# Kernel tuning notes

Hardware: AMD Instinct MI355X
Metric: run time of the kernel (lower is better)

## Reference

```python
import jax, jax.numpy as jnp
import numpy as np

EMBED = 2048
N_HEAD = 32
N_KV = 8
HEAD_DIM = 64
GROUP = N_HEAD // N_KV


def _rope_tables(seq_len, head_dim):
    inv_freq = 1.0 / (10000.0 ** (jnp.arange(0, head_dim, 2, dtype=jnp.float32) / head_dim))
    ang = jnp.arange(seq_len, dtype=jnp.float32)[:, None] * inv_freq[None, :]  # [S, D/2]
    ang = jnp.concatenate([ang, ang], axis=-1)  # [S, D]
    return jnp.cos(ang), jnp.sin(ang)


def apply_rope(x, cos, sin, offset=0):
    # x: [B, H, S, D]
    S, D = x.shape[2], x.shape[3]
    x1, x2 = x[..., : D // 2], x[..., D // 2 :]
    c = cos[offset : offset + S][None, None]
    s = sin[offset : offset + S][None, None]
    rotated = jnp.concatenate([-x2, x1], axis=-1)
    return (x * c + rotated * s).astype(x.dtype)


def setup_inputs() -> dict:
    key = jax.random.key(0)
    kx, kq, kk, kv, ko = jax.random.split(key, 5)
    B, S = 2, 2048
    x = jax.random.normal(kx, (B, S, EMBED), dtype=jnp.float32)
    mask = jnp.triu(jnp.ones((S, S), dtype=bool), k=1)  # causal: True = masked
    cos, sin = _rope_tables(S, HEAD_DIM)
    std = 0.02
    Wq = jax.random.normal(kq, (EMBED, EMBED), dtype=jnp.float32) * std
    Wk = jax.random.normal(kk, (EMBED, N_KV * HEAD_DIM), dtype=jnp.float32) * std
    Wv = jax.random.normal(kv, (EMBED, N_KV * HEAD_DIM), dtype=jnp.float32) * std
    Wo = jax.random.normal(ko, (EMBED, EMBED), dtype=jnp.float32) * std
    return {"x": x, "mask": mask, "cos": cos, "sin": sin,
            "Wq": Wq, "Wk": Wk, "Wv": Wv, "Wo": Wo}


def reference(x, mask, cos, sin, Wq, Wk, Wv, Wo):
    B, S, E = x.shape
    # projections (no bias)
    q = (x @ Wq).reshape(B, S, N_HEAD, HEAD_DIM).transpose(0, 2, 1, 3)  # [B,H,S,D]
    k = (x @ Wk).reshape(B, S, N_KV, HEAD_DIM).transpose(0, 2, 1, 3)    # [B,G,S,D]
    v = (x @ Wv).reshape(B, S, N_KV, HEAD_DIM).transpose(0, 2, 1, 3)    # [B,G,S,D]
    q = apply_rope(q, cos, sin, offset=0)
    k = apply_rope(k, cos, sin, offset=0)
    next_k, next_v = k, v  # kv cache to return
    # GQA: head h uses kv group h // GROUP; avoid repeat_interleave via reshape
    qg = q.reshape(B, N_KV, GROUP, S, HEAD_DIM)
    scores = jnp.einsum('bgjsd,bgtd->bgjst', qg, k) / np.float32(np.sqrt(HEAD_DIM))
    scores = jnp.where(mask[None, None, None], -jnp.inf, scores)
    attn = jax.nn.softmax(scores, axis=-1)
    out = jnp.einsum('bgjst,bgtd->bgjsd', attn, v)          # [B,G,group,S,D]
    out = out.reshape(B, N_HEAD, S, HEAD_DIM).transpose(0, 2, 1, 3).reshape(B, S, E)
    return out @ Wo, next_k, next_v
```

## Files before the change

kernel.cpp:

```cpp
#include <hip/hip_runtime.h>
#include <hip/hip_bf16.h>
#include <math.h>

#define NH 32
#define NKV 8
#define HD 64
#define B_ 2
#define S_ 2048
#define E_ 2048
#define M_ 4096

typedef unsigned short ushort_t;
typedef __attribute__((ext_vector_type(8))) short short8;
typedef __attribute__((ext_vector_type(4))) short short4v;
typedef __attribute__((ext_vector_type(4))) float floatx4;

__device__ inline unsigned short f2bf(float f) {
  unsigned int u = __float_as_uint(f);
  return (unsigned short)((u + 0x7FFFu + ((u >> 16) & 1u)) >> 16);
}

__device__ inline float fexp2(float x) {
  float r;
  asm("v_exp_f32 %0, %1" : "=v"(r) : "v"(x));
  return r;
}

__device__ inline void ld_lds16(const void* g, void* l) {
  __builtin_amdgcn_global_load_lds((__attribute__((address_space(1))) void*)g,
                                   (__attribute__((address_space(3))) void*)l, 16, 0, 0);
}

__global__ __launch_bounds__(256) void cast_x(const float* __restrict__ x,
                                              ushort_t* __restrict__ xb) {
  size_t i = ((size_t)blockIdx.x * 256 + threadIdx.x) * 8;
  float4 a = *(const float4*)(x + i);
  float4 b = *(const float4*)(x + i + 4);
  short8 o;
  o[0] = (short)f2bf(a.x); o[1] = (short)f2bf(a.y);
  o[2] = (short)f2bf(a.z); o[3] = (short)f2bf(a.w);
  o[4] = (short)f2bf(b.x); o[5] = (short)f2bf(b.y);
  o[6] = (short)f2bf(b.z); o[7] = (short)f2bf(b.w);
  *(short8*)(xb + i) = o;
}

__global__ __launch_bounds__(256) void transpose_w(const float* __restrict__ in,
                                                   ushort_t* __restrict__ out,
                                                   int R, int C) {
  __shared__ float tile[32][33];
  int c0 = blockIdx.x * 32, r0 = blockIdx.y * 32;
  int x = threadIdx.x, y0 = threadIdx.y;
  for (int i = 0; i < 4; i++) {
    int r = y0 + i * 8;
    tile[r][x] = in[(size_t)(r0 + r) * C + c0 + x];
  }
  __syncthreads();
  for (int i = 0; i < 4; i++) {
    int r = y0 + i * 8;
    out[(size_t)(c0 + r) * R + r0 + x] = f2bf(tile[x][r]);
  }
}

__global__ __launch_bounds__(256) void transpose_v(const float* __restrict__ outv,
                                                   ushort_t* __restrict__ vt) {
  __shared__ float t64[64][65];
  int bg = blockIdx.y;
  int tt = blockIdx.x;
  int s0 = tt * 64;
  int tid = threadIdx.x;
  size_t ibase = (size_t)bg * S_ * HD + (size_t)s0 * HD;
  for (int i = tid; i < 1024; i += 256) {
    int sr = i >> 4, dc = (i & 15) * 4;
    float4 v = *(const float4*)(outv + ibase + (size_t)sr * HD + dc);
    t64[sr][dc] = v.x; t64[sr][dc + 1] = v.y; t64[sr][dc + 2] = v.z; t64[sr][dc + 3] = v.w;
  }
  __syncthreads();
  size_t obase = ((size_t)bg * 32 + tt) * 4096;
  for (int i = tid; i < 512; i += 256) {
    int d = i >> 3, ss = (i & 7) * 8;
    short8 o;
#pragma unroll
    for (int e = 0; e < 8; e++) o[e] = (short)f2bf(t64[ss + e][d]);
    *(short8*)(vt + obase + d * 64 + (ss ^ ((d & 7) << 3))) = o;
  }
}

__device__ __forceinline__ void gemm128_core(const ushort_t* __restrict__ Ag,
                                             const ushort_t* __restrict__ Bg,
                                             floatx4 (&acc)[4][4]) {
  __shared__ __align__(16) ushort_t As[2][128][64];
  __shared__ __align__(16) ushort_t Bs[2][128][64];
  int tid = threadIdx.x;
  int w = tid >> 6, lane = tid & 63;
  int wm = (w >> 1) * 64, wn = (w & 1) * 64;
  int lr = lane & 15, quad = lane >> 4;
  int sx = lr & 7;
  char* Asb = (char*)As;
  char* Bsb = (char*)Bs;

  size_t so[4];
#pragma unroll
  for (int s = 0; s < 4; s++)
    so[s] = (size_t)(w * 32 + s * 8 + (lane >> 3)) * 4096 + (size_t)(((lane & 7) ^ (lane >> 3)) * 16);
  const char* abase = (const char*)Ag;
  const char* bbase = (const char*)Bg;

#define STAGE128(buf, kt)                                          \
  do {                                                             \
    size_t ko = (size_t)(kt) * 128;                                \
    char* Ad = Asb + (buf) * 16384 + w * 4096;                     \
    char* Bd = Bsb + (buf) * 16384 + w * 4096;                     \
    _Pragma("unroll") for (int s = 0; s < 4; s++) {                \
      ld_lds16(abase + so[s] + ko, Ad + s * 1024);                 \
      ld_lds16(bbase + so[s] + ko, Bd + s * 1024);                 \
    }                                                              \
  } while (0)

  STAGE128(0, 0);
  __syncthreads();

  int cur = 0;
  for (int kt = 0; kt < 32; kt++) {
    if (kt < 31) STAGE128(cur ^ 1, kt + 1);
    const char* Ab = Asb + cur * 16384;
    const char* Bb = Bsb + cur * 16384;
    short8 af[4][2], bfr[4][2];
#pragma unroll
    for (int i = 0; i < 4; i++) {
      size_t rb = (size_t)(wm + i * 16 + lr) * 128;
#pragma unroll
      for (int ks = 0; ks < 2; ks++)
        af[i][ks] = *(const short8*)(Ab + rb + (((ks * 4 + quad) ^ sx) << 4));
    }
#pragma unroll
    for (int j = 0; j < 4; j++) {
      size_t rb = (size_t)(wn + j * 16 + lr) * 128;
#pragma unroll
      for (int ks = 0; ks < 2; ks++)
        bfr[j][ks] = *(const short8*)(Bb + rb + (((ks * 4 + quad) ^ sx) << 4));
    }
#pragma unroll
    for (int i = 0; i < 4; i++)
#pragma unroll
      for (int j = 0; j < 4; j++) {
        acc[i][j] = __builtin_amdgcn_mfma_f32_16x16x32_bf16(af[i][0], bfr[j][0], acc[i][j], 0, 0, 0);
        acc[i][j] = __builtin_amdgcn_mfma_f32_16x16x32_bf16(af[i][1], bfr[j][1], acc[i][j], 0, 0, 0);
      }
    __syncthreads();
    cur ^= 1;
  }
#undef STAGE128
}

__global__ __launch_bounds__(256) void gemm_qkv(const ushort_t* __restrict__ xb,
                                                const ushort_t* __restrict__ WT,
                                                ushort_t* __restrict__ qbf,
                                                float* __restrict__ outk,
                                                ushort_t* __restrict__ kbf,
                                                float* __restrict__ outv,
                                                const float* __restrict__ cosP,
                                                const float* __restrict__ sinP) {
  int o = blockIdx.y * 24 + blockIdx.x;
  int swz = (o & 7) * 96 + (o >> 3);
  int n0 = (swz % 24) * 128, m0 = (swz / 24) * 128;
  int tid = threadIdx.x;
  int w = tid >> 6, lane = tid & 63;
  int wm = (w >> 1) * 64, wn = (w & 1) * 64;
  int lr = lane & 15, quad = lane >> 4;

  floatx4 acc[4][4] = {};
  gemm128_core(xb + (size_t)m0 * 2048, WT + (size_t)n0 * 2048, acc);

  if (n0 < 2048) {
    const float QS = 0.125f * 1.4426950408889634f;
#pragma unroll
    for (int i = 0; i < 4; i++)
#pragma unroll
      for (int j = 0; j < 2; j++) {
        int d = j * 16 + lr;
#pragma unroll
        for (int r = 0; r < 4; r++) {
          int row = m0 + wm + i * 16 + quad * 4 + r;
          int s = row & (S_ - 1);
          float c = cosP[s * 64 + d], sn = sinP[s * 64 + d];
          float x1 = acc[i][j][r], x2 = acc[i][j + 2][r];
          size_t oo = (size_t)row * 2048 + n0 + wn + d;
          qbf[oo] = f2bf((x1 * c - x2 * sn) * QS);
          qbf[oo + 32] = f2bf((x2 * c + x1 * sn) * QS);
        }
      }
  } else if (n0 < 2560) {
    int h = (n0 - 2048 + wn) >> 6;
#pragma unroll
    for (int i = 0; i < 4; i++)
#pragma unroll
      for (int j = 0; j < 2; j++) {
        int d = j * 16 + lr;
#pragma unroll
        for (int r = 0; r < 4; r++) {
          int row = m0 + wm + i * 16 + quad * 4 + r;
          int s = row & (S_ - 1), b = row >> 11;
          float c = cosP[s * 64 + d], sn = sinP[s * 64 + d];
          float x1 = acc[i][j][r], x2 = acc[i][j + 2][r];
          float y1 = x1 * c - x2 * sn, y2 = x2 * c + x1 * sn;
          size_t rowb = ((size_t)(b * NKV + h) * S_ + s) * 64;
          int xr = (s & 7) << 3;
          outk[rowb + d] = y1; outk[rowb + d + 32] = y2;
          kbf[rowb + (d ^ xr)] = f2bf(y1);
          kbf[rowb + ((d + 32) ^ xr)] = f2bf(y2);
        }
      }
  } else {
    int h = (n0 - 2560 + wn) >> 6;
#pragma unroll
    for (int i = 0; i < 4; i++)
#pragma unroll
      for (int j = 0; j < 4; j++) {
        int d = j * 16 + lr;
#pragma unroll
        for (int r = 0; r < 4; r++) {
          int row = m0 + wm + i * 16 + quad * 4 + r;
          int s = row & (S_ - 1), b = row >> 11;
          outv[((size_t)(b * NKV + h) * S_ + s) * 64 + d] = acc[i][j][r];
        }
      }
  }
}

__global__ __launch_bounds__(256) void gemm_o(const ushort_t* __restrict__ ctx,
                                              const ushort_t* __restrict__ WoT,
                                              float* __restrict__ y) {
  int o = blockIdx.y * 16 + blockIdx.x;
  int swz = (o & 7) * 64 + (o >> 3);
  int n0 = (swz % 16) * 128, m0 = (swz / 16) * 128;
  int tid = threadIdx.x;
  int w = tid >> 6, lane = tid & 63;
  int wm = (w >> 1) * 64, wn = (w & 1) * 64;
  int lr = lane & 15, quad = lane >> 4;

  floatx4 acc[4][4] = {};
  gemm128_core(ctx + (size_t)m0 * 2048, WoT + (size_t)n0 * 2048, acc);

#pragma unroll
  for (int i = 0; i < 4; i++)
#pragma unroll
    for (int j = 0; j < 4; j++) {
      int row = m0 + wm + i * 16 + quad * 4;
      int col = n0 + wn + j * 16 + lr;
#pragma unroll
      for (int r = 0; r < 4; r++)
        y[(size_t)(row + r) * 2048 + col] = acc[i][j][r];
    }
}

__global__ __launch_bounds__(256, 4) void attn2(ushort_t* __restrict__ q,
                                                const ushort_t* __restrict__ k,
                                                const ushort_t* __restrict__ vt) {
  __shared__ __align__(16) ushort_t KV[2][2][64][64];
  __shared__ __align__(16) ushort_t Ps[4][16][64];
  int bh = blockIdx.x;
  int qt = 31 - blockIdx.y;
  int b = bh >> 5, h = bh & 31, g = h >> 2;
  int tid = threadIdx.x;
  int w = tid >> 6, lane = tid & 63;
  int lr = lane & 15, quad = lane >> 4;

  int qg = qt * 64 + w * 16 + lr;
  short8 aq0, aq1;
  {
    const ushort_t* qp = q + ((size_t)(b * S_ + qg) * NH + h) * HD;
    aq0 = *(const short8*)(qp + quad * 8);
    aq1 = *(const short8*)(qp + 32 + quad * 8);
  }
  floatx4 od[4] = {};
  float mi = -INFINITY, li = 0.f;

  const char* ksrc = (const char*)(k + (size_t)(b * NKV + g) * S_ * HD) + w * 2048 + lane * 16;
  const char* vsrc = (const char*)(vt + (size_t)(b * NKV + g) * S_ * HD) + w * 2048 + lane * 16;
  char* dB = (char*)&KV[0][0][0][0] + w * 2048;

  int sw = (lr & 7) << 4;
  int ro0 = (quad * 16) ^ sw;
  int ro1 = (64 + quad * 16) ^ sw;
  char* Pw = (char*)&Ps[0][0][0] + w * 2048;

  ld_lds16(ksrc, dB);
  ld_lds16(ksrc + 1024, dB + 1024);
  ld_lds16(vsrc, dB + 8192);
  ld_lds16(vsrc + 1024, dB + 8192 + 1024);
  asm volatile("s_waitcnt vmcnt(0)" ::: "memory");
  __syncthreads();

  int cur = 0;
  for (int t = 0; t <= qt; t++) {
    if (t < qt) {
      const char* kn = ksrc + (size_t)(t + 1) * 8192;
      const char* vn = vsrc + (size_t)(t + 1) * 8192;
      char* d = dB + (cur ^ 1) * 16384;
      ld_lds16(kn, d); ld_lds16(kn + 1024, d + 1024);
      ld_lds16(vn, d + 8192); ld_lds16(vn + 1024, d + 8192 + 1024);
    }
    const char* Kb = (const char*)&KV[cur][0][0][0];
    const char* Vb = (const char*)&KV[cur][1][0][0];
    floatx4 sc[4];
#pragma unroll
    for (int kn = 0; kn < 4; kn++) {
      short8 a0 = *(const short8*)(Kb + (kn * 16 + lr) * 128 + ro0);
      short8 a1 = *(const short8*)(Kb + (kn * 16 + lr) * 128 + ro1);
      floatx4 c = {};
      c = __builtin_amdgcn_mfma_f32_16x16x32_bf16(a0, aq0, c, 0, 0, 0);
      c = __builtin_amdgcn_mfma_f32_16x16x32_bf16(a1, aq1, c, 0, 0, 0);
      sc[kn] = c;
    }
    float pv[16];
#pragma unroll
    for (int kn = 0; kn < 4; kn++)
#pragma unroll
      for (int r = 0; r < 4; r++) pv[kn * 4 + r] = sc[kn][r];
    if (t == qt) {
#pragma unroll
      for (int e = 0; e < 16; e++) {
        int kg = t * 64 + (e >> 2) * 16 + quad * 4 + (e & 3);
        if (kg > qg) pv[e] = -INFINITY;
      }
    }
    float mx = pv[0];
#pragma unroll
    for (int e = 1; e < 16; e++) mx = fmaxf(mx, pv[e]);
    mx = fmaxf(mx, __shfl_xor(mx, 16));
    mx = fmaxf(mx, __shfl_xor(mx, 32));
    if (__any(mx > mi + 11.5f)) {
      float mn = fmaxf(mi, mx);
      float al = fexp2(mi - mn);
      li *= al;
#pragma unroll
      for (int dn = 0; dn < 4; dn++) {
        od[dn][0] *= al; od[dn][1] *= al; od[dn][2] *= al; od[dn][3] *= al;
      }
      mi = mn;
    }
    float ps = 0.f;
#pragma unroll
    for (int e = 0; e < 16; e++) {
      pv[e] = fexp2(pv[e] - mi);
      ps += pv[e];
    }
    ps += __shfl_xor(ps, 16);
    ps += __shfl_xor(ps, 32);
    li += ps;
#pragma unroll
    for (int kn = 0; kn < 4; kn++) {
      unsigned int u0, u1;
      asm("v_cvt_pk_bf16_f32 %0, %1, %2" : "=v"(u0) : "v"(pv[kn * 4 + 0]), "v"(pv[kn * 4 + 1]));
      asm("v_cvt_pk_bf16_f32 %0, %1, %2" : "=v"(u1) : "v"(pv[kn * 4 + 2]), "v"(pv[kn * 4 + 3]));
      uint2 uu; uu.x = u0; uu.y = u1;
      *(uint2*)(Pw + lr * 128 + ((kn * 32 + quad * 8) ^ sw)) = uu;
    }
    short8 pb0 = *(const short8*)(Pw + lr * 128 + ro0);
    short8 pb1 = *(const short8*)(Pw + lr * 128 + ro1);
#pragma unroll
    for (int dn = 0; dn < 4; dn++) {
      short8 va = *(const short8*)(Vb + (dn * 16 + lr) * 128 + ro0);
      short8 vb = *(const short8*)(Vb + (dn * 16 + lr) * 128 + ro1);
      od[dn] = __builtin_amdgcn_mfma_f32_16x16x32_bf16(va, pb0, od[dn], 0, 0, 0);
      od[dn] = __builtin_amdgcn_mfma_f32_16x16x32_bf16(vb, pb1, od[dn], 0, 0, 0);
    }
    asm volatile("s_waitcnt vmcnt(0)" ::: "memory");
    __syncthreads();
    cur ^= 1;
  }
  float inv = 1.f / li;
  ushort_t* outp = q + ((size_t)(b * S_ + qg) * NH + h) * HD;
#pragma unroll
  for (int dn = 0; dn < 4; dn++) {
    short4v u;
    u[0] = (short)f2bf(od[dn][0] * inv); u[1] = (short)f2bf(od[dn][1] * inv);
    u[2] = (short)f2bf(od[dn][2] * inv); u[3] = (short)f2bf(od[dn][3] * inv);
    *(short4v*)(outp + dn * 16 + quad * 4) = u;
  }
}

extern "C" void kernel_launch(void* const* d_in, const int* in_sizes, int n_in,
                              void* d_out, int out_size, void* d_ws, size_t ws_size,
                              hipStream_t stream) {
  const float* x = (const float*)d_in[0];
  const float* cosT = (const float*)d_in[2];
  const float* sinT = (const float*)d_in[3];
  const float* Wq = (const float*)d_in[4];
  const float* Wk = (const float*)d_in[5];
  const float* Wv = (const float*)d_in[6];
  const float* Wo = (const float*)d_in[7];

  char* ws = (char*)d_ws;
  ushort_t* WT = (ushort_t*)(ws);
  ushort_t* WoT = (ushort_t*)(ws + 12582912);
  ushort_t* xb = (ushort_t*)(ws + 20971520);
  ushort_t* qbf = (ushort_t*)(ws + 37748736);
  ushort_t* kbf = (ushort_t*)(ws + 54525952);
  ushort_t* vt = (ushort_t*)(ws + 58720256);

  float* y = (float*)d_out;
  float* outk = y + (size_t)M_ * E_;
  float* outv = outk + (size_t)B_ * NKV * S_ * HD;

  cast_x<<<dim3(4096), 256, 0, stream>>>(x, xb);
  transpose_w<<<dim3(64, 64), dim3(32, 8), 0, stream>>>(Wq, WT, 2048, 2048);
  transpose_w<<<dim3(16, 64), dim3(32, 8), 0, stream>>>(Wk, WT + 2048 * 2048, 2048, 512);
  transpose_w<<<dim3(16, 64), dim3(32, 8), 0, stream>>>(Wv, WT + 2560 * 2048, 2048, 512);
  transpose_w<<<dim3(64, 64), dim3(32, 8), 0, stream>>>(Wo, WoT, 2048, 2048);

  gemm_qkv<<<dim3(24, 32), 256, 0, stream>>>(xb, WT, qbf, outk, kbf, outv, cosT, sinT);
  transpose_v<<<dim3(32, 16), 256, 0, stream>>>(outv, vt);

  attn2<<<dim3(64, 32), 256, 0, stream>>>(qbf, kbf, vt);

  gemm_o<<<dim3(16, 32), 256, 0, stream>>>(qbf, WoT, y);
}
```

Measured before the change: 344.0 us.

## Merge prep kernels into one launch, regroup GEMM tiles per XCD, prioritize attention MFMAs

Fuses the x cast and the four weight transposes into a single prep kernel with a flat block index, removing four kernel launches and their gaps. Remaps GEMM tile indices so each XCD gets a contiguous 8xN block of output tiles, which is meant to improve L2 reuse of A and B panels. It also raises wave priority around the MFMA sections in the attention kernel to favour matrix issue over other waves. The changes are independent. The tile remap assumes grid sizes that divide evenly across the XCD groups.

After: 322.2 us. 1.07x faster.

```diff
diff --git a/kernel.cpp b/kernel.cpp
--- a/kernel.cpp
+++ b/kernel.cpp
@@ -31,25 +31,10 @@
                                    (__attribute__((address_space(3))) void*)l, 16, 0, 0);
 }
 
-__global__ __launch_bounds__(256) void cast_x(const float* __restrict__ x,
-                                              ushort_t* __restrict__ xb) {
-  size_t i = ((size_t)blockIdx.x * 256 + threadIdx.x) * 8;
-  float4 a = *(const float4*)(x + i);
-  float4 b = *(const float4*)(x + i + 4);
-  short8 o;
-  o[0] = (short)f2bf(a.x); o[1] = (short)f2bf(a.y);
-  o[2] = (short)f2bf(a.z); o[3] = (short)f2bf(a.w);
-  o[4] = (short)f2bf(b.x); o[5] = (short)f2bf(b.y);
-  o[6] = (short)f2bf(b.z); o[7] = (short)f2bf(b.w);
-  *(short8*)(xb + i) = o;
-}
-
-__global__ __launch_bounds__(256) void transpose_w(const float* __restrict__ in,
-                                                   ushort_t* __restrict__ out,
-                                                   int R, int C) {
-  __shared__ float tile[32][33];
-  int c0 = blockIdx.x * 32, r0 = blockIdx.y * 32;
-  int x = threadIdx.x, y0 = threadIdx.y;
+__device__ inline void transp32(const float* __restrict__ in, ushort_t* __restrict__ out,
+                                int R, int C, int bx, int by, int tid, float (*tile)[33]) {
+  int c0 = bx * 32, r0 = by * 32;
+  int x = tid & 31, y0 = tid >> 5;
   for (int i = 0; i < 4; i++) {
     int r = y0 + i * 8;
     tile[r][x] = in[(size_t)(r0 + r) * C + c0 + x];
@@ -59,6 +44,38 @@
     int r = y0 + i * 8;
     out[(size_t)(c0 + r) * R + r0 + x] = f2bf(tile[x][r]);
   }
+}
+
+__global__ __launch_bounds__(256) void prep(const float* __restrict__ x,
+                                            ushort_t* __restrict__ xb,
+                                            const float* __restrict__ Wq,
+                                            const float* __restrict__ Wk,
+                                            const float* __restrict__ Wv,
+                                            const float* __restrict__ Wo,
+                                            ushort_t* __restrict__ WT,
+                                            ushort_t* __restrict__ WoT) {
+  __shared__ float tile[32][33];
+  int bid = blockIdx.x, tid = threadIdx.x;
+  if (bid < 4096) {
+    size_t i = ((size_t)bid * 256 + tid) * 8;
+    float4 a = *(const float4*)(x + i);
+    float4 b = *(const float4*)(x + i + 4);
+    short8 o;
+    o[0] = (short)f2bf(a.x); o[1] = (short)f2bf(a.y);
+    o[2] = (short)f2bf(a.z); o[3] = (short)f2bf(a.w);
+    o[4] = (short)f2bf(b.x); o[5] = (short)f2bf(b.y);
+    o[6] = (short)f2bf(b.z); o[7] = (short)f2bf(b.w);
+    *(short8*)(xb + i) = o;
+    return;
+  }
+  bid -= 4096;
+  if (bid < 4096) { transp32(Wq, WT, 2048, 2048, bid & 63, bid >> 6, tid, tile); return; }
+  bid -= 4096;
+  if (bid < 1024) { transp32(Wk, WT + 2048 * 2048, 2048, 512, bid & 15, bid >> 4, tid, tile); return; }
+  bid -= 1024;
+  if (bid < 1024) { transp32(Wv, WT + 2560 * 2048, 2048, 512, bid & 15, bid >> 4, tid, tile); return; }
+  bid -= 1024;
+  transp32(Wo, WoT, 2048, 2048, bid & 63, bid >> 6, tid, tile);
 }
 
 __global__ __launch_bounds__(256) void transpose_v(const float* __restrict__ outv,
@@ -161,8 +178,10 @@
                                                 const float* __restrict__ cosP,
                                                 const float* __restrict__ sinP) {
   int o = blockIdx.y * 24 + blockIdx.x;
-  int swz = (o & 7) * 96 + (o >> 3);
-  int n0 = (swz % 24) * 128, m0 = (swz / 24) * 128;
+  int xcd = o & 7, i = o >> 3;
+  int mg = xcd >> 1, ng = xcd & 1;
+  int m0 = (mg * 8 + i / 12) * 128;
+  int n0 = (ng * 12 + i % 12) * 128;
   int tid = threadIdx.x;
   int w = tid >> 6, lane = tid & 63;
   int wm = (w >> 1) * 64, wn = (w & 1) * 64;
@@ -174,16 +193,16 @@
   if (n0 < 2048) {
     const float QS = 0.125f * 1.4426950408889634f;
 #pragma unroll
-    for (int i = 0; i < 4; i++)
+    for (int i2 = 0; i2 < 4; i2++)
 #pragma unroll
       for (int j = 0; j < 2; j++) {
         int d = j * 16 + lr;
 #pragma unroll
         for (int r = 0; r < 4; r++) {
-          int row = m0 + wm + i * 16 + quad * 4 + r;
+          int row = m0 + wm + i2 * 16 + quad * 4 + r;
           int s = row & (S_ - 1);
           float c = cosP[s * 64 + d], sn = sinP[s * 64 + d];
-          float x1 = acc[i][j][r], x2 = acc[i][j + 2][r];
+          float x1 = acc[i2][j][r], x2 = acc[i2][j + 2][r];
           size_t oo = (size_t)row * 2048 + n0 + wn + d;
           qbf[oo] = f2bf((x1 * c - x2 * sn) * QS);
           qbf[oo + 32] = f2bf((x2 * c + x1 * sn) * QS);
@@ -192,16 +211,16 @@
   } else if (n0 < 2560) {
     int h = (n0 - 2048 + wn) >> 6;
 #pragma unroll
-    for (int i = 0; i < 4; i++)
+    for (int i2 = 0; i2 < 4; i2++)
 #pragma unroll
       for (int j = 0; j < 2; j++) {
         int d = j * 16 + lr;
 #pragma unroll
         for (int r = 0; r < 4; r++) {
-          int row = m0 + wm + i * 16 + quad * 4 + r;
+          int row = m0 + wm + i2 * 16 + quad * 4 + r;
           int s = row & (S_ - 1), b = row >> 11;
           float c = cosP[s * 64 + d], sn = sinP[s * 64 + d];
-          float x1 = acc[i][j][r], x2 = acc[i][j + 2][r];
+          float x1 = acc[i2][j][r], x2 = acc[i2][j + 2][r];
           float y1 = x1 * c - x2 * sn, y2 = x2 * c + x1 * sn;
           size_t rowb = ((size_t)(b * NKV + h) * S_ + s) * 64;
           int xr = (s & 7) << 3;
@@ -213,15 +232,15 @@
   } else {
     int h = (n0 - 2560 + wn) >> 6;
 #pragma unroll
-    for (int i = 0; i < 4; i++)
+    for (int i2 = 0; i2 < 4; i2++)
 #pragma unroll
       for (int j = 0; j < 4; j++) {
         int d = j * 16 + lr;
 #pragma unroll
         for (int r = 0; r < 4; r++) {
-          int row = m0 + wm + i * 16 + quad * 4 + r;
+          int row = m0 + wm + i2 * 16 + quad * 4 + r;
           int s = row & (S_ - 1), b = row >> 11;
-          outv[((size_t)(b * NKV + h) * S_ + s) * 64 + d] = acc[i][j][r];
+          outv[((size_t)(b * NKV + h) * S_ + s) * 64 + d] = acc[i2][j][r];
         }
       }
   }
@@ -231,8 +250,10 @@
                                               const ushort_t* __restrict__ WoT,
                                               float* __restrict__ y) {
   int o = blockIdx.y * 16 + blockIdx.x;
-  int swz = (o & 7) * 64 + (o >> 3);
-  int n0 = (swz % 16) * 128, m0 = (swz / 16) * 128;
+  int xcd = o & 7, i = o >> 3;
+  int mg = xcd >> 1, ng = xcd & 1;
+  int m0 = (mg * 8 + (i >> 3)) * 128;
+  int n0 = (ng * 8 + (i & 7)) * 128;
   int tid = threadIdx.x;
   int w = tid >> 6, lane = tid & 63;
   int wm = (w >> 1) * 64, wn = (w & 1) * 64;
@@ -242,14 +263,14 @@
   gemm128_core(ctx + (size_t)m0 * 2048, WoT + (size_t)n0 * 2048, acc);
 
 #pragma unroll
-  for (int i = 0; i < 4; i++)
+  for (int i2 = 0; i2 < 4; i2++)
 #pragma unroll
     for (int j = 0; j < 4; j++) {
-      int row = m0 + wm + i * 16 + quad * 4;
+      int row = m0 + wm + i2 * 16 + quad * 4;
       int col = n0 + wn + j * 16 + lr;
 #pragma unroll
       for (int r = 0; r < 4; r++)
-        y[(size_t)(row + r) * 2048 + col] = acc[i][j][r];
+        y[(size_t)(row + r) * 2048 + col] = acc[i2][j][r];
     }
 }
 
@@ -303,6 +324,7 @@
     const char* Kb = (const char*)&KV[cur][0][0][0];
     const char* Vb = (const char*)&KV[cur][1][0][0];
     floatx4 sc[4];
+    __builtin_amdgcn_s_setprio(1);
 #pragma unroll
     for (int kn = 0; kn < 4; kn++) {
       short8 a0 = *(const short8*)(Kb + (kn * 16 + lr) * 128 + ro0);
@@ -312,6 +334,7 @@
       c = __builtin_amdgcn_mfma_f32_16x16x32_bf16(a1, aq1, c, 0, 0, 0);
       sc[kn] = c;
     }
+    __builtin_amdgcn_s_setprio(0);
     float pv[16];
 #pragma unroll
     for (int kn = 0; kn < 4; kn++)
@@ -358,6 +381,7 @@
     }
     short8 pb0 = *(const short8*)(Pw + lr * 128 + ro0);
     short8 pb1 = *(const short8*)(Pw + lr * 128 + ro1);
+    __builtin_amdgcn_s_setprio(1);
 #pragma unroll
     for (int dn = 0; dn < 4; dn++) {
       short8 va = *(const short8*)(Vb + (dn * 16 + lr) * 128 + ro0);
@@ -365,6 +389,7 @@
       od[dn] = __builtin_amdgcn_mfma_f32_16x16x32_bf16(va, pb0, od[dn], 0, 0, 0);
       od[dn] = __builtin_amdgcn_mfma_f32_16x16x32_bf16(vb, pb1, od[dn], 0, 0, 0);
     }
+    __builtin_amdgcn_s_setprio(0);
     asm volatile("s_waitcnt vmcnt(0)" ::: "memory");
     __syncthreads();
     cur ^= 1;
@@ -403,11 +428,7 @@
   float* outk = y + (size_t)M_ * E_;
   float* outv = outk + (size_t)B_ * NKV * S_ * HD;
 
-  cast_x<<<dim3(4096), 256, 0, stream>>>(x, xb);
-  transpose_w<<<dim3(64, 64), dim3(32, 8), 0, stream>>>(Wq, WT, 2048, 2048);
-  transpose_w<<<dim3(16, 64), dim3(32, 8), 0, stream>>>(Wk, WT + 2048 * 2048, 2048, 512);
-  transpose_w<<<dim3(16, 64), dim3(32, 8), 0, stream>>>(Wv, WT + 2560 * 2048, 2048, 512);
-  transpose_w<<<dim3(64, 64), dim3(32, 8), 0, stream>>>(Wo, WoT, 2048, 2048);
+  prep<<<dim3(14336), 256, 0, stream>>>(x, xb, Wq, Wk, Wv, Wo, WT, WoT);
 
   gemm_qkv<<<dim3(24, 32), 256, 0, stream>>>(xb, WT, qbf, outk, kbf, outv, cosT, sinT);
   transpose_v<<<dim3(32, 16), 256, 0, stream>>>(outv, vt);
```
